# Optimization experiments

Hardware: AMD Instinct MI355X
Metric: run time of the kernel (lower is better)

## Reference

```python
import jax, jax.numpy as jnp
import numpy as np

KSIZE = 7
NSPIX = 196


def _unfold(x, k):
    # x: (T, C, H, W) -> (T, C, k*k, H, W), reflect padding, torch Unfold ordering
    p = (k - 1) // 2
    T, C, H, W = x.shape
    xp = jnp.pad(x, ((0, 0), (0, 0), (p, p), (p, p)), mode='reflect')
    return jnp.stack([xp[:, :, i:i + H, j:j + W] for i in range(k) for j in range(k)], axis=2)


def setup_inputs() -> dict:
    key = jax.random.key(0)
    k1, k2, k3, k4, k5 = jax.random.split(key, 5)
    T, C, H, W = 2, 64, 160, 160
    fan_in = C * KSIZE * KSIZE
    x = jax.random.normal(k1, (T, C, H, W), jnp.float32)
    spix = jax.random.randint(k2, (T, H, W), 0, NSPIX, jnp.int32)
    W_lin = jax.random.normal(k3, (C, fan_in), jnp.float32) / np.sqrt(fan_in)
    b_lin = jax.random.normal(k4, (C,), jnp.float32) * 0.01
    w_scale = jax.random.normal(k5, (C,), jnp.float32) / np.sqrt(C)
    b_scale = jnp.zeros((1,), jnp.float32)
    return {"x": x, "spix": spix, "W_lin": W_lin, "b_lin": b_lin,
            "w_scale": w_scale, "b_scale": b_scale}


def reference(x, spix, W_lin, b_lin, w_scale, b_scale):
    T, C, H, W = x.shape
    K2 = KSIZE * KSIZE
    O = W_lin.shape[0]
    p = (KSIZE - 1) // 2

    # unfold(x) with reflect padding -> patches (T, C, K2, H, W)
    patches = _unfold(x, KSIZE)

    # unfold(spix) -> neighbor superpixel ids per pixel (T, K2, H, W)
    sp = jnp.pad(spix, ((0, 0), (p, p), (p, p)), mode='reflect')
    nb = jnp.stack([sp[:, i:i + H, j:j + W] for i in range(KSIZE) for j in range(KSIZE)], axis=1)

    # per-frame superpixel mean pooling (bist.get_pooled_video): down (T, S, C)
    seg = (spix.astype(jnp.int32) + jnp.arange(T, dtype=jnp.int32)[:, None, None] * NSPIX).reshape(-1)
    feats = x.transpose(0, 2, 3, 1).reshape(-1, C)  # (T*H*W, C)
    sums = jax.ops.segment_sum(feats, seg, num_segments=T * NSPIX).reshape(T, NSPIX, C)
    cnts = jax.ops.segment_sum(jnp.ones((seg.shape[0],), x.dtype), seg,
                               num_segments=T * NSPIX).reshape(T, NSPIX, 1)
    down = sums / jnp.maximum(cnts, 1.0)

    # squared pairwise distances between superpixel means: pwd (T, S, S)
    sq = jnp.sum(down * down, axis=-1)
    pwd = jnp.maximum(sq[:, :, None] + sq[:, None, :]
                      - 2.0 * jnp.einsum('tsc,tuc->tsu', down, down), 0.0)

    # sims[t,k,h,w] = ||mean(spix[t,h,w]) - mean(nb[t,k,h,w])||^2
    tidx = jnp.arange(T)[:, None, None, None]
    sims = pwd[tidx, spix[:, None, :, :], nb]  # (T, K2, H, W)

    # scale = 10 * softplus(1x1-conv(x / ||x||_c))  -> (T, H, W)
    xn = x / (jnp.linalg.norm(x, axis=1, keepdims=True) + 1e-10)
    scale = 10.0 * jax.nn.softplus(jnp.einsum('c,tchw->thw', w_scale, xn) + b_scale[0])

    # apply_norm 'exp_max' over the kernel-tap axis
    rw = jnp.exp(-scale[:, None, :, :] * sims)  # (T, K2, H, W)
    rw = rw / (1e-5 + jnp.max(rw, axis=1, keepdims=True))

    # dynamic conv: out[t,o,h,w] = sum_{c,k} W[o,c,k] * patches[t,c,k,h,w] * rw[t,k,h,w] + b[o]
    out = jnp.einsum('ock,tckhw,tkhw->tohw', W_lin.reshape(O, C, K2), patches, rw)
    return out + b_lin[None, :, None, None]
```

## Files before the change

### kernel.cpp

```cpp
#include <hip/hip_runtime.h>
#include <math.h>

#define TT 2
#define CC 64
#define HH 160
#define WW 160
#define KS 7
#define K2 49
#define NSPIX 196
#define HWSZ (HH*WW)
#define PAD 3
#define OO 64
#define FANIN (CC*K2)
#define TS 8
#define PS (TS+KS-1)
#define NPOS (PS*PS)

#define NCHUNK 50
#define CHUNKPIX 512
#define NCG 8

typedef short short8 __attribute__((ext_vector_type(8)));
typedef float f32x16 __attribute__((ext_vector_type(16)));

__device__ __forceinline__ int reflect(int i, int n) {
    if (i < 0) i = -i;
    if (i >= n) i = 2*n - 2 - i;
    return i;
}

__device__ __forceinline__ unsigned short f2bf(float f) {
    unsigned int u = __float_as_uint(f);
    unsigned int r = (u + 0x7FFFu + ((u >> 16) & 1u)) >> 16;
    return (unsigned short)r;
}
__device__ __forceinline__ float bf2f(unsigned short s) {
    return __uint_as_float(((unsigned int)s) << 16);
}

__global__ __launch_bounds__(256) void k_prep(const float* __restrict__ x,
                                              const int* __restrict__ spix,
                                              const float* __restrict__ Wl,
                                              const float* __restrict__ wsc,
                                              const float* __restrict__ bsc,
                                              float* __restrict__ partials,
                                              float* __restrict__ cntp,
                                              float* __restrict__ scale,
                                              unsigned short* __restrict__ Wb) {
    __shared__ float ls[8*200];
    __shared__ float lcnt[200];
    int bid = blockIdx.x;
    int tid = threadIdx.x;

    if (bid < 800) {
        int cg = bid & 7;
        int rest = bid >> 3;
        int ch = rest % NCHUNK;
        int t  = rest / NCHUNK;

        for (int i = tid; i < 8*200; i += 256) ls[i] = 0.f;
        if (cg == 0) for (int i = tid; i < 200; i += 256) lcnt[i] = 0.f;
        __syncthreads();

        int base = ch*CHUNKPIX;
        const float* xb = x + ((size_t)t*CC + cg*8)*HWSZ;
        #pragma unroll
        for (int i = 0; i < CHUNKPIX; i += 256) {
            int pix = base + i + tid;
            int s = spix[t*HWSZ + pix];
            if (cg == 0) atomicAdd(&lcnt[s], 1.0f);
            #pragma unroll
            for (int j = 0; j < 8; ++j) atomicAdd(&ls[j*200 + s], xb[(size_t)j*HWSZ + pix]);
        }
        __syncthreads();

        float* pb = partials + ((size_t)(t*NCHUNK + ch)*NSPIX)*CC + cg*8;
        for (int i = tid; i < 8*NSPIX; i += 256) {
            int s = i >> 3, j = i & 7;
            pb[s*CC + j] = ls[j*200 + s];
        }
        if (cg == 0)
            for (int i = tid; i < NSPIX; i += 256)
                cntp[(t*NCHUNK + ch)*NSPIX + i] = lcnt[i];
    } else if (bid < 1000) {
        int pix = (bid - 800)*256 + tid;
        if (pix < TT*HWSZ) {
            int t = pix / HWSZ, hw = pix - t*HWSZ;
            const float* xs = x + (size_t)t*CC*HWSZ + hw;
            float s1 = 0.f, s2 = 0.f;
            #pragma unroll 8
            for (int c = 0; c < CC; ++c) { float v = xs[c*HWSZ]; s1 += wsc[c]*v; s2 += v*v; }
            float z = s1/(sqrtf(s2) + 1e-10f) + bsc[0];
            float sp_ = (z > 0.f) ? z + log1pf(expf(-z)) : log1pf(expf(z));
            scale[pix] = 10.f*sp_;
        }
    } else {
        int row = (bid - 1000)*256 + tid;
        if (row < 2*K2*4*64) {
            int ln  = row & 63;
            int kc  = (row >> 6) & 3;
            int tq  = row >> 8;
            int tap = tq % K2;
            int qo  = tq / K2;
            int o = qo*32 + (ln & 31);
            int cb = kc*16 + (ln >> 5)*8;
            unsigned short* dst = Wb + (size_t)row*8;
            const float* src = Wl + (size_t)o*FANIN + tap;
            #pragma unroll
            for (int j = 0; j < 8; ++j) dst[j] = f2bf(src[(size_t)(cb + j)*K2]);
        }
    }
}

__global__ __launch_bounds__(256) void k_red(const float* __restrict__ partials,
                                             const float* __restrict__ cntp,
                                             float* __restrict__ down,
                                             float* __restrict__ sq) {
    int ts = blockIdx.x*4 + threadIdx.y;
    if (ts >= TT*NSPIX) return;
    int t = ts / NSPIX, s = ts - t*NSPIX;
    int c = threadIdx.x;

    const float* pb = partials + ((size_t)t*NCHUNK*NSPIX + s)*CC + c;
    float acc = 0.f;
    #pragma unroll 10
    for (int ch = 0; ch < NCHUNK; ++ch) acc += pb[(size_t)ch*NSPIX*CC];

    float cv = (c < NCHUNK) ? cntp[(t*NCHUNK + c)*NSPIX + s] : 0.f;
    #pragma unroll
    for (int off = 1; off < 64; off <<= 1) cv += __shfl_xor(cv, off, 64);

    float d = acc / fmaxf(cv, 1.0f);
    down[ts*CC + c] = d;
    float v = d*d;
    #pragma unroll
    for (int off = 1; off < 64; off <<= 1) v += __shfl_xor(v, off, 64);
    if (c == 0) sq[ts] = v;
}

__global__ void k_pwd(const float* __restrict__ down, const float* __restrict__ sq,
                      float* __restrict__ pwd) {
    int tid = blockIdx.x*256 + threadIdx.x;
    if (tid >= TT*NSPIX*NSPIX) return;
    int t = tid / (NSPIX*NSPIX); int r = tid - t*NSPIX*NSPIX;
    int s = r / NSPIX, u = r - (r / NSPIX)*NSPIX;
    const float* ds = down + (t*NSPIX + s)*CC;
    const float* du = down + (t*NSPIX + u)*CC;
    float dot = 0.f;
    #pragma unroll 4
    for (int c = 0; c < CC; ++c) dot += ds[c]*du[c];
    float v = sq[t*NSPIX + s] + sq[t*NSPIX + u] - 2.f*dot;
    pwd[tid] = fmaxf(v, 0.f);
}

__global__ __launch_bounds__(256, 4) void k_main(
    const float* __restrict__ x, const int* __restrict__ spix,
    const unsigned short* __restrict__ Wb, const float* __restrict__ b_lin,
    const float* __restrict__ pwd, const float* __restrict__ scale,
    float* __restrict__ out)
{
    __shared__ unsigned short xpT[NPOS*64];
    __shared__ unsigned short rwb[K2*64];
    __shared__ int   sp[NPOS];
    __shared__ float mxp[4*64];
    __shared__ float mxl[64];

    int bid = blockIdx.x;
    int t = bid / 400;
    int r = bid - t*400;
    int th0 = (r / 20)*TS, tw0 = (r - (r/20)*20)*TS;
    int tid = threadIdx.y*64 + threadIdx.x;

    for (int i = tid; i < NPOS; i += 256) {
        int rr = reflect(th0 + i/PS - PAD, HH);
        int cc = reflect(tw0 + i%PS - PAD, WW);
        sp[i] = spix[t*HWSZ + rr*WW + cc];
    }
    for (int i = tid; i < NPOS*32; i += 256) {
        int pos = i % NPOS;
        int cp  = i / NPOS;
        int rr = reflect(th0 + pos/PS - PAD, HH);
        int cc = reflect(tw0 + pos%PS - PAD, WW);
        const float* xs = x + ((size_t)t*CC + 2*cp)*HWSZ + rr*WW + cc;
        float v0 = xs[0];
        float v1 = xs[HWSZ];
        unsigned int pk = (unsigned int)f2bf(v0) | ((unsigned int)f2bf(v1) << 16);
        int idx = pos*64 + (((cp >> 2) ^ (pos & 7)) << 3) + (cp & 3)*2;
        *(unsigned int*)&xpT[idx] = pk;
    }
    __syncthreads();

    int p_ = threadIdx.x;
    int ty = threadIdx.y;
    int py0 = p_ >> 3, px0 = p_ & 7;
    {
        float sc = scale[t*HWSZ + (th0 + py0)*WW + (tw0 + px0)];
        int s0 = sp[(py0 + PAD)*PS + (px0 + PAD)];
        const float* pr = pwd + (t*NSPIX + s0)*NSPIX;
        float pmax = 0.f;
        for (int k = ty; k < K2; k += 4) {
            int di = k/KS, dj = k - di*KS;
            int nb = sp[(py0 + di)*PS + (px0 + dj)];
            float v = expf(-sc * pr[nb]);
            rwb[k*64 + p_] = f2bf(v);
            pmax = fmaxf(pmax, v);
        }
        mxp[ty*64 + p_] = pmax;
    }
    __syncthreads();
    if (ty == 0) {
        float m = fmaxf(fmaxf(mxp[p_], mxp[64 + p_]), fmaxf(mxp[128 + p_], mxp[192 + p_]));
        mxl[p_] = 1.f/(1e-5f + m);
    }
    __syncthreads();
    {
        float s = mxl[p_];
        for (int k = ty; k < K2; k += 4)
            rwb[k*64 + p_] = f2bf(bf2f(rwb[k*64 + p_]) * s);
    }
    __syncthreads();

    int ln = threadIdx.x;
    int wv = __builtin_amdgcn_readfirstlane(threadIdx.y);
    int qp = wv & 1, kh = wv >> 1;
    int p  = qp*32 + (ln & 31);
    int ppy = p >> 3, ppx = p & 7;
    int kc0 = 2*kh, kc1 = 2*kh + 1;
    int lhi = ln >> 5;

    const unsigned short* A00b = Wb + (size_t)kc0*512 + ln*8;
    const unsigned short* A10b = A00b + (size_t)K2*4*512;

    f32x16 Czero;
    #pragma unroll
    for (int i = 0; i < 16; ++i) Czero[i] = 0.f;
    f32x16 acc0 = Czero, acc1 = Czero;

    int jc0 = 2*kc0 + lhi, jc1 = 2*kc1 + lhi;

    int di = 0, dj = 0;
    #pragma unroll 7
    for (int tap = 0; tap < K2; ++tap) {
        const unsigned short* a0 = A00b + tap*2048;
        short8 A00 = *(const short8*)(a0);
        short8 A01 = *(const short8*)(a0 + 512);
        const unsigned short* a1 = A10b + tap*2048;
        short8 A10 = *(const short8*)(a1);
        short8 A11 = *(const short8*)(a1 + 512);

        int pos = (ppy + di)*PS + (ppx + dj);
        int sw  = pos & 7;
        const unsigned short* bbase = &xpT[pos*64];
        short8 B0 = *(const short8*)(bbase + ((jc0 ^ sw) << 3));
        short8 B1 = *(const short8*)(bbase + ((jc1 ^ sw) << 3));

        f32x16 C0 = __builtin_amdgcn_mfma_f32_32x32x16_bf16(A00, B0, Czero, 0, 0, 0);
        C0 = __builtin_amdgcn_mfma_f32_32x32x16_bf16(A01, B1, C0, 0, 0, 0);
        f32x16 C1 = __builtin_amdgcn_mfma_f32_32x32x16_bf16(A10, B0, Czero, 0, 0, 0);
        C1 = __builtin_amdgcn_mfma_f32_32x32x16_bf16(A11, B1, C1, 0, 0, 0);

        float rwv = bf2f(rwb[tap*64 + p]);
        #pragma unroll
        for (int i = 0; i < 16; ++i) acc0[i] = fmaf(C0[i], rwv, acc0[i]);
        #pragma unroll
        for (int i = 0; i < 16; ++i) acc1[i] = fmaf(C1[i], rwv, acc1[i]);

        if (++dj == KS) { dj = 0; ++di; }
    }

    __syncthreads();
    float* red = (float*)xpT;
    if (kh == 1) {
        #pragma unroll
        for (int i = 0; i < 16; ++i) {
            red[i*128 + qp*64 + ln]        = acc0[i];
            red[(16 + i)*128 + qp*64 + ln] = acc1[i];
        }
    }
    __syncthreads();
    if (kh == 0) {
        int h = th0 + ppy, w = tw0 + ppx;
        int row_hi = 4*lhi;
        float* ob = out + (size_t)t*OO*HWSZ + h*WW + w;
        #pragma unroll
        for (int rg = 0; rg < 16; ++rg) {
            float v0 = acc0[rg] + red[rg*128 + qp*64 + ln];
            float v1 = acc1[rg] + red[(16 + rg)*128 + qp*64 + ln];
            int o0 = (rg & 3) + 8*(rg >> 2) + row_hi;
            int o1 = 32 + o0;
            ob[(size_t)o0*HWSZ] = v0 + b_lin[o0];
            ob[(size_t)o1*HWSZ] = v1 + b_lin[o1];
        }
    }
}

extern "C" void kernel_launch(void* const* d_in, const int* in_sizes, int n_in,
                              void* d_out, int out_size, void* d_ws, size_t ws_size,
                              hipStream_t stream) {
    const float* x    = (const float*)d_in[0];
    const int*   spix = (const int*)d_in[1];
    const float* Wl   = (const float*)d_in[2];
    const float* bl   = (const float*)d_in[3];
    const float* wsc  = (const float*)d_in[4];
    const float* bsc  = (const float*)d_in[5];
    float* out = (float*)d_out;

    float* ws    = (float*)d_ws;
    float* down  = ws;
    float* sq    = down + TT*NSPIX*CC;
    float* pwd   = sq   + TT*NSPIX;
    float* scale = pwd  + TT*NSPIX*NSPIX;
    float* cntp  = scale + TT*HWSZ;
    float* parts = cntp + TT*NCHUNK*NSPIX;
    unsigned short* Wb = (unsigned short*)(parts + (size_t)TT*NCHUNK*NSPIX*CC);

    k_prep<<<1196, 256, 0, stream>>>(x, spix, Wl, wsc, bsc, parts, cntp, scale, Wb);
    {
        dim3 blk(64, 4, 1);
        k_red <<<(TT*NSPIX + 3)/4, blk, 0, stream>>>(parts, cntp, down, sq);
    }
    k_pwd <<<(TT*NSPIX*NSPIX + 255)/256, 256, 0, stream>>>(down, sq, pwd);

    dim3 blk(64, 4, 1);
    k_main<<<TT*(HH/TS)*(WW/TS), blk, 0, stream>>>(x, spix, Wb, bl, pwd, scale, out);
}
```

Before: 162.5 us.

## Split reweighting computation into separate kernel and stage bf16 weights in global

Moves the per-tile superpixel similarity and exp-max normalisation out of the main conv kernel into a new k_rw kernel. That kernel writes normalised bf16 weights per tile into workspace, reusing the parts buffer. k_main now only loads the x patch and copies the precomputed weights, which removes three barriers and the gather/exp work from its critical path. The cost is an extra launch and a global round trip for the weights. It also drops a double bf16 rounding, so normalisation now runs in fp32 before rounding.

```diff
diff --git a/kernel.cpp b/kernel.cpp
--- a/kernel.cpp
+++ b/kernel.cpp
@@ -18,7 +18,6 @@
 
 #define NCHUNK 50
 #define CHUNKPIX 512
-#define NCG 8
 
 typedef short short8 __attribute__((ext_vector_type(8)));
 typedef float f32x16 __attribute__((ext_vector_type(16)));
@@ -153,15 +152,12 @@
     pwd[tid] = fmaxf(v, 0.f);
 }
 
-__global__ __launch_bounds__(256, 4) void k_main(
-    const float* __restrict__ x, const int* __restrict__ spix,
-    const unsigned short* __restrict__ Wb, const float* __restrict__ b_lin,
-    const float* __restrict__ pwd, const float* __restrict__ scale,
-    float* __restrict__ out)
-{
-    __shared__ unsigned short xpT[NPOS*64];
-    __shared__ unsigned short rwb[K2*64];
+__global__ __launch_bounds__(256) void k_rw(const int* __restrict__ spix,
+                                            const float* __restrict__ pwd,
+                                            const float* __restrict__ scale,
+                                            unsigned short* __restrict__ rw_g) {
     __shared__ int   sp[NPOS];
+    __shared__ float rwt[K2*64];
     __shared__ float mxp[4*64];
     __shared__ float mxl[64];
 
@@ -175,18 +171,6 @@
         int rr = reflect(th0 + i/PS - PAD, HH);
         int cc = reflect(tw0 + i%PS - PAD, WW);
         sp[i] = spix[t*HWSZ + rr*WW + cc];
-    }
-    for (int i = tid; i < NPOS*32; i += 256) {
-        int pos = i % NPOS;
-        int cp  = i / NPOS;
-        int rr = reflect(th0 + pos/PS - PAD, HH);
-        int cc = reflect(tw0 + pos%PS - PAD, WW);
-        const float* xs = x + ((size_t)t*CC + 2*cp)*HWSZ + rr*WW + cc;
-        float v0 = xs[0];
-        float v1 = xs[HWSZ];
-        unsigned int pk = (unsigned int)f2bf(v0) | ((unsigned int)f2bf(v1) << 16);
-        int idx = pos*64 + (((cp >> 2) ^ (pos & 7)) << 3) + (cp & 3)*2;
-        *(unsigned int*)&xpT[idx] = pk;
     }
     __syncthreads();
 
@@ -202,7 +186,7 @@
             int di = k/KS, dj = k - di*KS;
             int nb = sp[(py0 + di)*PS + (px0 + dj)];
             float v = expf(-sc * pr[nb]);
-            rwb[k*64 + p_] = f2bf(v);
+            rwt[k*64 + p_] = v;
             pmax = fmaxf(pmax, v);
         }
         mxp[ty*64 + p_] = pmax;
@@ -213,10 +197,47 @@
         mxl[p_] = 1.f/(1e-5f + m);
     }
     __syncthreads();
+    unsigned int* dst = (unsigned int*)(rw_g + (size_t)bid*K2*64);
+    for (int i = tid; i < K2*32; i += 256) {
+        int k = i >> 5;
+        int pp = (i & 31)*2;
+        float v0 = rwt[k*64 + pp]     * mxl[pp];
+        float v1 = rwt[k*64 + pp + 1] * mxl[pp + 1];
+        dst[i] = (unsigned int)f2bf(v0) | ((unsigned int)f2bf(v1) << 16);
+    }
+}
+
+__global__ __launch_bounds__(256, 4) void k_main(
+    const float* __restrict__ x,
+    const unsigned short* __restrict__ Wb, const float* __restrict__ b_lin,
+    const unsigned short* __restrict__ rw_g,
+    float* __restrict__ out)
+{
+    __shared__ unsigned short xpT[NPOS*64];
+    __shared__ unsigned short rwb[K2*64];
+
+    int bid = blockIdx.x;
+    int t = bid / 400;
+    int r = bid - t*400;
+    int th0 = (r / 20)*TS, tw0 = (r - (r/20)*20)*TS;
+    int tid = threadIdx.y*64 + threadIdx.x;
+
+    for (int i = tid; i < NPOS*32; i += 256) {
+        int pos = i % NPOS;
+        int cp  = i / NPOS;
+        int rr = reflect(th0 + pos/PS - PAD, HH);
+        int cc = reflect(tw0 + pos%PS - PAD, WW);
+        const float* xs = x + ((size_t)t*CC + 2*cp)*HWSZ + rr*WW + cc;
+        float v0 = xs[0];
+        float v1 = xs[HWSZ];
+        unsigned int pk = (unsigned int)f2bf(v0) | ((unsigned int)f2bf(v1) << 16);
+        int idx = pos*64 + (((cp >> 2) ^ (pos & 7)) << 3) + (cp & 3)*2;
+        *(unsigned int*)&xpT[idx] = pk;
+    }
     {
-        float s = mxl[p_];
-        for (int k = ty; k < K2; k += 4)
-            rwb[k*64 + p_] = f2bf(bf2f(rwb[k*64 + p_]) * s);
+        const unsigned int* src = (const unsigned int*)(rw_g + (size_t)bid*K2*64);
+        unsigned int* d = (unsigned int*)rwb;
+        for (int i = tid; i < K2*32; i += 256) d[i] = src[i];
     }
     __syncthreads();
 
@@ -313,6 +334,7 @@
     float* cntp  = scale + TT*HWSZ;
     float* parts = cntp + TT*NCHUNK*NSPIX;
     unsigned short* Wb = (unsigned short*)(parts + (size_t)TT*NCHUNK*NSPIX*CC);
+    unsigned short* rw_g = (unsigned short*)parts;
 
     k_prep<<<1196, 256, 0, stream>>>(x, spix, Wl, wsc, bsc, parts, cntp, scale, Wb);
     {
@@ -320,7 +342,11 @@
         k_red <<<(TT*NSPIX + 3)/4, blk, 0, stream>>>(parts, cntp, down, sq);
     }
     k_pwd <<<(TT*NSPIX*NSPIX + 255)/256, 256, 0, stream>>>(down, sq, pwd);
+    {
+        dim3 blk(64, 4, 1);
+        k_rw  <<<TT*400, blk, 0, stream>>>(spix, pwd, scale, rw_g);
+    }
 
     dim3 blk(64, 4, 1);
-    k_main<<<TT*(HH/TS)*(WW/TS), blk, 0, stream>>>(x, spix, Wb, bl, pwd, scale, out);
-}
+    k_main<<<TT*400, blk, 0, stream>>>(x, Wb, bl, rw_g, out);
+}
```

Result: slower. 169.4 us (+4.2%).

## Fold superpixel reduction into atomics, drop reduce kernel, remap MFMA wave tiling

Applied to the files above, without the earlier changes.

Per-chunk partial sums are now added straight into global superpixel sums and counts with atomics, after a memset. This removes the separate reduction kernel and the large partials buffer. The pairwise-distance kernel computes means on the fly and takes the direct squared difference, which also changes numerics slightly. In the main kernel each wave now holds one output half for two pixel halves, so it loads two A fragments and four B fragments per tap instead of four A and two B, moving weight traffic from global memory to LDS. The cost is global atomic contention and an extra memset launch.

```diff
diff --git a/kernel.cpp b/kernel.cpp
--- a/kernel.cpp
+++ b/kernel.cpp
@@ -18,7 +18,6 @@
 
 #define NCHUNK 50
 #define CHUNKPIX 512
-#define NCG 8
 
 typedef short short8 __attribute__((ext_vector_type(8)));
 typedef float f32x16 __attribute__((ext_vector_type(16)));
@@ -43,8 +42,8 @@
                                               const float* __restrict__ Wl,
                                               const float* __restrict__ wsc,
                                               const float* __restrict__ bsc,
-                                              float* __restrict__ partials,
-                                              float* __restrict__ cntp,
+                                              float* __restrict__ sums,
+                                              float* __restrict__ cnts,
                                               float* __restrict__ scale,
                                               unsigned short* __restrict__ Wb) {
     __shared__ float ls[8*200];
@@ -74,14 +73,17 @@
         }
         __syncthreads();
 
-        float* pb = partials + ((size_t)(t*NCHUNK + ch)*NSPIX)*CC + cg*8;
+        float* sb = sums + (size_t)t*NSPIX*CC + cg*8;
         for (int i = tid; i < 8*NSPIX; i += 256) {
             int s = i >> 3, j = i & 7;
-            pb[s*CC + j] = ls[j*200 + s];
+            float v = ls[j*200 + s];
+            if (v != 0.f) atomicAdd(&sb[s*CC + j], v);
         }
         if (cg == 0)
-            for (int i = tid; i < NSPIX; i += 256)
-                cntp[(t*NCHUNK + ch)*NSPIX + i] = lcnt[i];
+            for (int i = tid; i < NSPIX; i += 256) {
+                float v = lcnt[i];
+                if (v != 0.f) atomicAdd(&cnts[t*NSPIX + i], v);
+            }
     } else if (bid < 1000) {
         int pix = (bid - 800)*256 + tid;
         if (pix < TT*HWSZ) {
@@ -112,45 +114,24 @@
     }
 }
 
-__global__ __launch_bounds__(256) void k_red(const float* __restrict__ partials,
-                                             const float* __restrict__ cntp,
-                                             float* __restrict__ down,
-                                             float* __restrict__ sq) {
-    int ts = blockIdx.x*4 + threadIdx.y;
-    if (ts >= TT*NSPIX) return;
-    int t = ts / NSPIX, s = ts - t*NSPIX;
-    int c = threadIdx.x;
-
-    const float* pb = partials + ((size_t)t*NCHUNK*NSPIX + s)*CC + c;
-    float acc = 0.f;
-    #pragma unroll 10
-    for (int ch = 0; ch < NCHUNK; ++ch) acc += pb[(size_t)ch*NSPIX*CC];
-
-    float cv = (c < NCHUNK) ? cntp[(t*NCHUNK + c)*NSPIX + s] : 0.f;
-    #pragma unroll
-    for (int off = 1; off < 64; off <<= 1) cv += __shfl_xor(cv, off, 64);
-
-    float d = acc / fmaxf(cv, 1.0f);
-    down[ts*CC + c] = d;
-    float v = d*d;
-    #pragma unroll
-    for (int off = 1; off < 64; off <<= 1) v += __shfl_xor(v, off, 64);
-    if (c == 0) sq[ts] = v;
-}
-
-__global__ void k_pwd(const float* __restrict__ down, const float* __restrict__ sq,
-                      float* __restrict__ pwd) {
+__global__ __launch_bounds__(256) void k_pwd(const float* __restrict__ sums,
+                                             const float* __restrict__ cnts,
+                                             float* __restrict__ pwd) {
     int tid = blockIdx.x*256 + threadIdx.x;
     if (tid >= TT*NSPIX*NSPIX) return;
     int t = tid / (NSPIX*NSPIX); int r = tid - t*NSPIX*NSPIX;
     int s = r / NSPIX, u = r - (r / NSPIX)*NSPIX;
-    const float* ds = down + (t*NSPIX + s)*CC;
-    const float* du = down + (t*NSPIX + u)*CC;
-    float dot = 0.f;
-    #pragma unroll 4
-    for (int c = 0; c < CC; ++c) dot += ds[c]*du[c];
-    float v = sq[t*NSPIX + s] + sq[t*NSPIX + u] - 2.f*dot;
-    pwd[tid] = fmaxf(v, 0.f);
+    const float* ds = sums + (size_t)(t*NSPIX + s)*CC;
+    const float* du = sums + (size_t)(t*NSPIX + u)*CC;
+    float is = 1.0f / fmaxf(cnts[t*NSPIX + s], 1.0f);
+    float iu = 1.0f / fmaxf(cnts[t*NSPIX + u], 1.0f);
+    float acc = 0.f;
+    #pragma unroll 8
+    for (int c = 0; c < CC; ++c) {
+        float d = ds[c]*is - du[c]*iu;
+        acc = fmaf(d, d, acc);
+    }
+    pwd[tid] = acc;
 }
 
 __global__ __launch_bounds__(256, 4) void k_main(
@@ -222,48 +203,49 @@
 
     int ln = threadIdx.x;
     int wv = __builtin_amdgcn_readfirstlane(threadIdx.y);
-    int qp = wv & 1, kh = wv >> 1;
-    int p  = qp*32 + (ln & 31);
-    int ppy = p >> 3, ppx = p & 7;
-    int kc0 = 2*kh, kc1 = 2*kh + 1;
+    int qo = wv & 1, kh = wv >> 1;
     int lhi = ln >> 5;
-
-    const unsigned short* A00b = Wb + (size_t)kc0*512 + ln*8;
-    const unsigned short* A10b = A00b + (size_t)K2*4*512;
+    int l31 = ln & 31;
+    int p0 = l31, p1 = 32 + l31;
+    int ppy0 = p0 >> 3, ppx0 = p0 & 7;
+
+    int kc0 = 2*kh;
+    int jc0 = 4*kh + lhi, jc1 = 4*kh + 2 + lhi;
+
+    const unsigned short* Ab = Wb + ((size_t)(qo*K2*4) + kc0)*512 + ln*8;
 
     f32x16 Czero;
     #pragma unroll
     for (int i = 0; i < 16; ++i) Czero[i] = 0.f;
     f32x16 acc0 = Czero, acc1 = Czero;
 
-    int jc0 = 2*kc0 + lhi, jc1 = 2*kc1 + lhi;
-
     int di = 0, dj = 0;
     #pragma unroll 7
     for (int tap = 0; tap < K2; ++tap) {
-        const unsigned short* a0 = A00b + tap*2048;
-        short8 A00 = *(const short8*)(a0);
-        short8 A01 = *(const short8*)(a0 + 512);
-        const unsigned short* a1 = A10b + tap*2048;
-        short8 A10 = *(const short8*)(a1);
-        short8 A11 = *(const short8*)(a1 + 512);
-
-        int pos = (ppy + di)*PS + (ppx + dj);
-        int sw  = pos & 7;
-        const unsigned short* bbase = &xpT[pos*64];
-        short8 B0 = *(const short8*)(bbase + ((jc0 ^ sw) << 3));
-        short8 B1 = *(const short8*)(bbase + ((jc1 ^ sw) << 3));
-
-        f32x16 C0 = __builtin_amdgcn_mfma_f32_32x32x16_bf16(A00, B0, Czero, 0, 0, 0);
-        C0 = __builtin_amdgcn_mfma_f32_32x32x16_bf16(A01, B1, C0, 0, 0, 0);
-        f32x16 C1 = __builtin_amdgcn_mfma_f32_32x32x16_bf16(A10, B0, Czero, 0, 0, 0);
-        C1 = __builtin_amdgcn_mfma_f32_32x32x16_bf16(A11, B1, C1, 0, 0, 0);
-
-        float rwv = bf2f(rwb[tap*64 + p]);
-        #pragma unroll
-        for (int i = 0; i < 16; ++i) acc0[i] = fmaf(C0[i], rwv, acc0[i]);
-        #pragma unroll
-        for (int i = 0; i < 16; ++i) acc1[i] = fmaf(C1[i], rwv, acc1[i]);
+        const unsigned short* a = Ab + (size_t)tap*2048;
+        short8 A0 = *(const short8*)(a);
+        short8 A1 = *(const short8*)(a + 512);
+
+        int pos0 = (ppy0 + di)*PS + (ppx0 + dj);
+        int sw   = pos0 & 7;
+        const unsigned short* b0 = &xpT[pos0*64];
+        const unsigned short* b1 = b0 + 56*64;
+        short8 B00 = *(const short8*)(b0 + ((jc0 ^ sw) << 3));
+        short8 B01 = *(const short8*)(b0 + ((jc1 ^ sw) << 3));
+        short8 B10 = *(const short8*)(b1 + ((jc0 ^ sw) << 3));
+        short8 B11 = *(const short8*)(b1 + ((jc1 ^ sw) << 3));
+
+        f32x16 C0 = __builtin_amdgcn_mfma_f32_32x32x16_bf16(A0, B00, Czero, 0, 0, 0);
+        C0 = __builtin_amdgcn_mfma_f32_32x32x16_bf16(A1, B01, C0, 0, 0, 0);
+        f32x16 C1 = __builtin_amdgcn_mfma_f32_32x32x16_bf16(A0, B10, Czero, 0, 0, 0);
+        C1 = __builtin_amdgcn_mfma_f32_32x32x16_bf16(A1, B11, C1, 0, 0, 0);
+
+        float rwv0 = bf2f(rwb[tap*64 + p0]);
+        float rwv1 = bf2f(rwb[tap*64 + p1]);
+        #pragma unroll
+        for (int i = 0; i < 16; ++i) acc0[i] = fmaf(C0[i], rwv0, acc0[i]);
+        #pragma unroll
+        for (int i = 0; i < 16; ++i) acc1[i] = fmaf(C1[i], rwv1, acc1[i]);
 
         if (++dj == KS) { dj = 0; ++di; }
     }
@@ -273,23 +255,24 @@
     if (kh == 1) {
         #pragma unroll
         for (int i = 0; i < 16; ++i) {
-            red[i*128 + qp*64 + ln]        = acc0[i];
-            red[(16 + i)*128 + qp*64 + ln] = acc1[i];
+            red[((qo*2 + 0)*16 + i)*64 + ln] = acc0[i];
+            red[((qo*2 + 1)*16 + i)*64 + ln] = acc1[i];
         }
     }
     __syncthreads();
     if (kh == 0) {
-        int h = th0 + ppy, w = tw0 + ppx;
+        int h0 = th0 + ppy0, w0 = tw0 + ppx0;
         int row_hi = 4*lhi;
-        float* ob = out + (size_t)t*OO*HWSZ + h*WW + w;
+        float* ob0 = out + (size_t)t*OO*HWSZ + h0*WW + w0;
+        float* ob1 = ob0 + 4*WW;
         #pragma unroll
         for (int rg = 0; rg < 16; ++rg) {
-            float v0 = acc0[rg] + red[rg*128 + qp*64 + ln];
-            float v1 = acc1[rg] + red[(16 + rg)*128 + qp*64 + ln];
-            int o0 = (rg & 3) + 8*(rg >> 2) + row_hi;
-            int o1 = 32 + o0;
-            ob[(size_t)o0*HWSZ] = v0 + b_lin[o0];
-            ob[(size_t)o1*HWSZ] = v1 + b_lin[o1];
+            int o = qo*32 + (rg & 3) + 8*(rg >> 2) + row_hi;
+            float v0 = acc0[rg] + red[((qo*2 + 0)*16 + rg)*64 + ln];
+            float v1 = acc1[rg] + red[((qo*2 + 1)*16 + rg)*64 + ln];
+            float bl = b_lin[o];
+            ob0[(size_t)o*HWSZ] = v0 + bl;
+            ob1[(size_t)o*HWSZ] = v1 + bl;
         }
     }
 }
@@ -306,21 +289,17 @@
     float* out = (float*)d_out;
 
     float* ws    = (float*)d_ws;
-    float* down  = ws;
-    float* sq    = down + TT*NSPIX*CC;
-    float* pwd   = sq   + TT*NSPIX;
+    float* sums  = ws;
+    float* cnts  = sums + TT*NSPIX*CC;
+    float* pwd   = cnts + TT*NSPIX;
     float* scale = pwd  + TT*NSPIX*NSPIX;
-    float* cntp  = scale + TT*HWSZ;
-    float* parts = cntp + TT*NCHUNK*NSPIX;
-    unsigned short* Wb = (unsigned short*)(parts + (size_t)TT*NCHUNK*NSPIX*CC);
-
-    k_prep<<<1196, 256, 0, stream>>>(x, spix, Wl, wsc, bsc, parts, cntp, scale, Wb);
-    {
-        dim3 blk(64, 4, 1);
-        k_red <<<(TT*NSPIX + 3)/4, blk, 0, stream>>>(parts, cntp, down, sq);
-    }
-    k_pwd <<<(TT*NSPIX*NSPIX + 255)/256, 256, 0, stream>>>(down, sq, pwd);
+    unsigned short* Wb = (unsigned short*)(scale + TT*HWSZ);
+
+    hipMemsetAsync(sums, 0, (size_t)(TT*NSPIX*CC + TT*NSPIX)*sizeof(float), stream);
+
+    k_prep<<<1196, 256, 0, stream>>>(x, spix, Wl, wsc, bsc, sums, cnts, scale, Wb);
+    k_pwd <<<(TT*NSPIX*NSPIX + 255)/256, 256, 0, stream>>>(sums, cnts, pwd);
 
     dim3 blk(64, 4, 1);
-    k_main<<<TT*(HH/TS)*(WW/TS), blk, 0, stream>>>(x, spix, Wb, bl, pwd, scale, out);
-}
+    k_main<<<TT*400, blk, 0, stream>>>(x, spix, Wb, bl, pwd, scale, out);
+}
```

Result: faster. 159.1 us (-2.1%).
